# Kernel optimization log

Hardware: AMD Instinct MI355X
Metric: run time of the kernel (lower is better)

Reference implementation:

```python
import jax, jax.numpy as jnp
import numpy as np

EPS = 1e-18
MARGIN = 0.2  # hp.margin (cancels: positive/positive == 1)
BIAS = 1.0    # hp.bias


def setup_inputs() -> dict:
    key = jax.random.key(0)
    k1, k2, k3, k4 = jax.random.split(key, 4)
    B, T, D = 32, 256, 256  # T == D required by the broadcast in Ecos_sim
    return {
        "pre_VF": jax.random.normal(k1, (B, T, D), dtype=jnp.float32),
        "pre_AF": jax.random.normal(k2, (B, T, D), dtype=jnp.float32),
        "back_VF": jax.random.normal(k3, (B, T, D), dtype=jnp.float32),
        "back_AF": jax.random.normal(k4, (B, T, D), dtype=jnp.float32),
    }


def _direction_loss(V, A):
    """For each anchor i: log(1 + sum_{j != i} exp(sim(V_i, A_j))).

    sim(V_i, A_j)[t, s] = (V_i @ A_j.T)[t, s] / (||V_i||_F * colnorm(A_j)[s])
    (faithful to Ecos_sim: scalar Frobenius norm for V, per-column norm for A,
    broadcast along the last axis; positive/positive == 1 exactly, so the
    positive term and margin cancel.)
    """
    B = V.shape[0]
    # upper[i,j,t,s] = <V[i,t,:], A[j,s,:]>
    upper = jnp.einsum("itd,jsd->ijts", V, A)
    v_norm = jnp.sqrt(jnp.sum(V ** 2, axis=(1, 2)) + EPS)      # [B]
    a_norm = jnp.sqrt(jnp.sum(A ** 2, axis=1) + EPS)           # [B, D]
    sim = upper / (v_norm[:, None, None, None] * a_norm[None, :, None, :])
    e_sim = jnp.exp(sim)                                        # [B,B,T,T]
    idx = jnp.arange(B)
    down = e_sim.sum(axis=1) - e_sim[idx, idx]                  # exclude j == i
    rows = jnp.log(1.0 + down)                                  # [B,T,T]
    return rows.reshape(-1, rows.shape[-1])                     # cat along dim 0


def reference(pre_VF, pre_AF, back_VF, back_AF):
    sim_back_V = _direction_loss(back_VF, back_AF)
    sim_back_A = _direction_loss(back_AF, back_VF)
    return -(1.0 / BIAS) * (sim_back_V + sim_back_A)
```

## Files before the change

kernel.cpp:

```cpp
#include <hip/hip_runtime.h>
#include <cstdint>

#define R_TOT 8192
#define KD    256
#define SLOT  ((size_t)R_TOT * KD)
#define IVN_OFF  0
#define ICN_OFF  256
#define CSQ_OFF  (ICN_OFF + 65536)
#define MATS_OFF (CSQ_OFF + 524288)

typedef float f32x4 __attribute__((ext_vector_type(4)));
typedef int   i32x4 __attribute__((ext_vector_type(4)));
typedef int   i32x8 __attribute__((ext_vector_type(8)));

__device__ __forceinline__ void glds16(const void* g, void* l){
  __builtin_amdgcn_global_load_lds((const __attribute__((address_space(1))) uint32_t*)g,
                                   (__attribute__((address_space(3))) uint32_t*)l, 16, 0, 0);
}

__global__ void cast_ns_k(const float* __restrict__ V, const float* __restrict__ A,
                          unsigned char* __restrict__ mats, float* __restrict__ csq){
  const int tc = blockIdx.x, j = blockIdx.y, ten = blockIdx.z;
  const int tid = threadIdx.x;
  const int g    = tid & 31;
  const int tsub = tid >> 5;
  const int c    = g >> 1;
  const int half = g & 1;
  const float* X = (ten ? A : V) + (size_t)j * 65536;
  unsigned char* M = mats + (size_t)ten * SLOT + (size_t)j * 65536;
  float cs[8];
  #pragma unroll
  for (int e = 0; e < 8; ++e) cs[e] = 0.f;
  #pragma unroll
  for (int tt = 0; tt < 4; ++tt){
    const int t = tc * 32 + tt * 8 + tsub;
    const float4 p0 = *(const float4*)(X + t * 256 + g * 8);
    const float4 p1 = *(const float4*)(X + t * 256 + g * 8 + 4);
    cs[0] += p0.x * p0.x; cs[1] += p0.y * p0.y; cs[2] += p0.z * p0.z; cs[3] += p0.w * p0.w;
    cs[4] += p1.x * p1.x; cs[5] += p1.y * p1.y; cs[6] += p1.z * p1.z; cs[7] += p1.w * p1.w;
    int d0 = __builtin_amdgcn_cvt_pk_fp8_f32(p0.x, p0.y, 0, false);
    d0     = __builtin_amdgcn_cvt_pk_fp8_f32(p0.z, p0.w, d0, true);
    int d1 = __builtin_amdgcn_cvt_pk_fp8_f32(p1.x, p1.y, 0, false);
    d1     = __builtin_amdgcn_cvt_pk_fp8_f32(p1.z, p1.w, d1, true);
    int2 o; o.x = d0; o.y = d1;
    *(int2*)(M + (size_t)t * 256 + (((c ^ (t & 15)) << 4) | (half << 3))) = o;
  }
  __shared__ float red[8][256];
  #pragma unroll
  for (int e = 0; e < 8; ++e) red[tsub][g * 8 + e] = cs[e];
  __syncthreads();
  float s = 0.f;
  #pragma unroll
  for (int gg = 0; gg < 8; ++gg) s += red[gg][tid];
  csq[(size_t)((tc * 2 + ten) * 32 + j) * 256 + tid] = s;
}

__global__ void nreduce_k(const float* __restrict__ csq, float* __restrict__ ivn,
                          float* __restrict__ icn){
  const int j = blockIdx.x, ten = blockIdx.y, s = threadIdx.x;
  float c = 0.f;
  #pragma unroll
  for (int tc = 0; tc < 8; ++tc)
    c += csq[(size_t)((tc * 2 + ten) * 32 + j) * 256 + s];
  icn[ten * 8192 + j * 256 + s] = rsqrtf(c + 1e-18f);
  __shared__ float red[256];
  red[s] = c; __syncthreads();
  for (int off = 128; off > 0; off >>= 1){
    if (s < off) red[s] += red[s + off];
    __syncthreads();
  }
  if (s == 0) ivn[ten * 32 + j] = rsqrtf(red[0] + 1e-18f);
}

__global__ __launch_bounds__(512, 4) void gemm_both_k(const unsigned char* __restrict__ mats,
                                                      const float* __restrict__ ivn,
                                                      const float* __restrict__ icn,
                                                      float* __restrict__ out){
  __shared__ __align__(16) char smem[40960];
  const int tid  = threadIdx.x;
  const int lane = tid & 63;
  const int w    = tid >> 6;
  const int dir  = w >> 2;
  const int sub  = w & 3;
  const int lm   = lane & 15;
  const int kh   = lane >> 4;
  const int s0   = blockIdx.x * 16;
  const int rb   = blockIdx.y;
  const int r0   = rb * 256;
  const int ib   = rb;

  const unsigned char* rowmat = mats + (size_t)dir * SLOT;
  const unsigned char* colmat = mats + (size_t)(1 - dir) * SLOT;
  const float sivn = ivn[dir * 32 + ib] * 1.44269504088896340736f;

  char*  dbase = smem + dir * 16384;
  float* cscw  = (float*)(smem + 32768) + dir * 512;
  const unsigned char* colbase = colmat + (size_t)s0 * 256;
  const int lo16 = lane * 16;

  auto issue = [&](int x){
    const int j = x + (x >= ib ? 1 : 0);
    glds16(colbase + (size_t)j * 65536 + sub * 1024 + lo16,
           dbase + ((x & 3) << 12) + sub * 1024 + lo16);
  };

  issue(0);
  issue(1);

  {
    const float* ib2 = icn + (size_t)(1 - dir) * 8192 + s0 + lm;
    #pragma unroll
    for (int jx = 0; jx < 2; ++jx){
      const int j = sub * 8 + jx * 4 + kh;
      cscw[j * 16 + lm] = sivn * ib2[j * 256];
    }
  }

  i32x8 afr[4][2];
  #pragma unroll
  for (int mi = 0; mi < 4; ++mi){
    const unsigned char* rp = rowmat + (size_t)(r0 + sub * 64 + mi * 16 + lm) * 256;
    #pragma unroll
    for (int t = 0; t < 2; ++t){
      i32x4 lo = *(const i32x4*)(rp + ((((t << 3) | (kh << 1) | 0) ^ lm) << 4));
      i32x4 hi = *(const i32x4*)(rp + ((((t << 3) | (kh << 1) | 1) ^ lm) << 4));
      afr[mi][t] = i32x8{lo.x, lo.y, lo.z, lo.w, hi.x, hi.y, hi.z, hi.w};
    }
  }
  #pragma unroll
  for (int mi = 0; mi < 4; ++mi)
    #pragma unroll
    for (int t = 0; t < 2; ++t)
      asm volatile("" : "+v"(afr[mi][t]));

  int ad[2][2];
  #pragma unroll
  for (int t = 0; t < 2; ++t)
    #pragma unroll
    for (int u = 0; u < 2; ++u)
      ad[t][u] = lm * 256 + ((((t << 3) | (kh << 1) | u) ^ lm) << 4);

  f32x4 acc[4];
  #pragma unroll
  for (int mi = 0; mi < 4; ++mi)
    acc[mi] = f32x4{0.f, 0.f, 0.f, 0.f};
  const f32x4 fz = {0.f, 0.f, 0.f, 0.f};

  asm volatile("s_waitcnt vmcnt(0) lgkmcnt(0)" ::: "memory");
  __builtin_amdgcn_s_barrier();
  __builtin_amdgcn_sched_barrier(0);

  #pragma unroll 1
  for (int x = 0; x < 31; ++x){
    const int j = x + (x >= ib ? 1 : 0);

    if (x <= 28) issue(x + 2);

    const char* rbuf = dbase + ((x & 3) << 12);
    i32x8 b[2];
    #pragma unroll
    for (int t = 0; t < 2; ++t){
      i32x4 lo = *(const i32x4*)(rbuf + ad[t][0]);
      i32x4 hi = *(const i32x4*)(rbuf + ad[t][1]);
      b[t] = i32x8{lo.x, lo.y, lo.z, lo.w, hi.x, hi.y, hi.z, hi.w};
    }
    const float csc = cscw[j * 16 + lm];

    f32x4 S[4];
    #pragma unroll
    for (int mi = 0; mi < 4; ++mi)
      S[mi] = __builtin_amdgcn_mfma_scale_f32_16x16x128_f8f6f4(afr[mi][0], b[0], fz, 0, 0, 0, 127, 0, 127);
    #pragma unroll
    for (int mi = 0; mi < 4; ++mi)
      S[mi] = __builtin_amdgcn_mfma_scale_f32_16x16x128_f8f6f4(afr[mi][1], b[1], S[mi], 0, 0, 0, 127, 0, 127);

    #pragma unroll
    for (int mi = 0; mi < 4; ++mi){
      const f32x4 t0 = S[mi] * csc;
      f32x4 e0;
      #pragma unroll
      for (int r = 0; r < 4; ++r) e0[r] = __builtin_amdgcn_exp2f(t0[r]);
      acc[mi] += e0;
    }

    if (x <= 28)      asm volatile("s_waitcnt vmcnt(1)" ::: "memory");
    else if (x == 29) asm volatile("s_waitcnt vmcnt(0)" ::: "memory");
    if (x < 30){
      __builtin_amdgcn_s_barrier();
      __builtin_amdgcn_sched_barrier(0);
    }
  }

  __syncthreads();
  float* ebuf = (float*)smem;
  #pragma unroll
  for (int mi = 0; mi < 4; ++mi){
    #pragma unroll
    for (int r = 0; r < 4; ++r){
      const int m = sub * 64 + mi * 16 + (kh << 2) + r;
      ebuf[(dir * 256 + m) * 20 + lm] = __logf(1.f + acc[mi][r]);
    }
  }
  __syncthreads();
  #pragma unroll
  for (int p = 0; p < 2; ++p){
    const int i   = tid + p * 512;
    const int row = i >> 2;
    const int c4  = i & 3;
    const f32x4 e0 = *(const f32x4*)(&ebuf[row * 20 + c4 * 4]);
    const f32x4 e1 = *(const f32x4*)(&ebuf[(256 + row) * 20 + c4 * 4]);
    f32x4 o;
    #pragma unroll
    for (int e = 0; e < 4; ++e) o[e] = -(e0[e] + e1[e]);
    *(f32x4*)(&out[(size_t)(r0 + row) * 256 + s0 + c4 * 4]) = o;
  }
}

extern "C" void kernel_launch(void* const* d_in, const int* in_sizes, int n_in,
                              void* d_out, int out_size, void* d_ws, size_t ws_size,
                              hipStream_t stream){
  const float* V = (const float*)d_in[2];
  const float* A = (const float*)d_in[3];
  float* out = (float*)d_out;
  float* ivn = (float*)((char*)d_ws + IVN_OFF);
  float* icn = (float*)((char*)d_ws + ICN_OFF);
  float* csq = (float*)((char*)d_ws + CSQ_OFF);
  unsigned char* mats = (unsigned char*)((char*)d_ws + MATS_OFF);

  cast_ns_k<<<dim3(8, 32, 2), 256, 0, stream>>>(V, A, mats, csq);
  nreduce_k<<<dim3(32, 2), 256, 0, stream>>>(csq, ivn, icn);
  gemm_both_k<<<dim3(16, 32), 512, 0, stream>>>(mats, ivn, icn, out);
}
```

Before: 115.0 us.

## Deepen LDS ring to eight stages and process two column tiles per barrier

The shared-memory ring for column tiles grows from 4 to 8 slots, and four tiles are prefetched instead of two. The main loop now handles two tiles per iteration, with one barrier and waitcnt per pair. Within a pair, the second tile's MFMAs are interleaved with the first tile's exp/accumulate to hide latency. The cost is a larger LDS footprint (about 68KB per block), which lowers the number of blocks that can be resident per CU.

```diff
diff --git a/kernel.cpp b/kernel.cpp
--- a/kernel.cpp
+++ b/kernel.cpp
@@ -76,7 +76,7 @@
                                                       const float* __restrict__ ivn,
                                                       const float* __restrict__ icn,
                                                       float* __restrict__ out){
-  __shared__ __align__(16) char smem[40960];
+  __shared__ __align__(16) char smem[69632];
   const int tid  = threadIdx.x;
   const int lane = tid & 63;
   const int w    = tid >> 6;
@@ -93,19 +93,18 @@
   const unsigned char* colmat = mats + (size_t)(1 - dir) * SLOT;
   const float sivn = ivn[dir * 32 + ib] * 1.44269504088896340736f;
 
-  char*  dbase = smem + dir * 16384;
-  float* cscw  = (float*)(smem + 32768) + dir * 512;
+  char*  dbase = smem + dir * 32768;
+  float* cscw  = (float*)(smem + 65536) + dir * 512;
   const unsigned char* colbase = colmat + (size_t)s0 * 256;
   const int lo16 = lane * 16;
 
   auto issue = [&](int x){
     const int j = x + (x >= ib ? 1 : 0);
     glds16(colbase + (size_t)j * 65536 + sub * 1024 + lo16,
-           dbase + ((x & 3) << 12) + sub * 1024 + lo16);
+           dbase + ((x & 7) << 12) + sub * 1024 + lo16);
   };
 
-  issue(0);
-  issue(1);
+  issue(0); issue(1); issue(2); issue(3);
 
   {
     const float* ib2 = icn + (size_t)(1 - dir) * 8192 + s0 + lm;
@@ -150,46 +149,77 @@
   __builtin_amdgcn_s_barrier();
   __builtin_amdgcn_sched_barrier(0);
 
+#define RD(RX, BUF) do{                                                         \
+    i32x4 lo0_ = *(const i32x4*)((BUF) + ad[0][0]);                             \
+    i32x4 hi0_ = *(const i32x4*)((BUF) + ad[0][1]);                             \
+    i32x4 lo1_ = *(const i32x4*)((BUF) + ad[1][0]);                             \
+    i32x4 hi1_ = *(const i32x4*)((BUF) + ad[1][1]);                             \
+    RX[0] = i32x8{lo0_.x, lo0_.y, lo0_.z, lo0_.w, hi0_.x, hi0_.y, hi0_.z, hi0_.w}; \
+    RX[1] = i32x8{lo1_.x, lo1_.y, lo1_.z, lo1_.w, hi1_.x, hi1_.y, hi1_.z, hi1_.w}; \
+  }while(0)
+
+#define MFMA8(SX, BX) do{                                                       \
+    _Pragma("unroll")                                                           \
+    for (int mi_ = 0; mi_ < 4; ++mi_)                                           \
+      SX[mi_] = __builtin_amdgcn_mfma_scale_f32_16x16x128_f8f6f4(afr[mi_][0], BX[0], fz, 0, 0, 0, 127, 0, 127); \
+    _Pragma("unroll")                                                           \
+    for (int mi_ = 0; mi_ < 4; ++mi_)                                           \
+      SX[mi_] = __builtin_amdgcn_mfma_scale_f32_16x16x128_f8f6f4(afr[mi_][1], BX[1], SX[mi_], 0, 0, 0, 127, 0, 127); \
+  }while(0)
+
+#define EXPACC(SX, CY) do{                                                      \
+    _Pragma("unroll")                                                           \
+    for (int mi_ = 0; mi_ < 4; ++mi_){                                          \
+      const f32x4 t_ = SX[mi_] * (CY);                                          \
+      f32x4 e_;                                                                 \
+      _Pragma("unroll")                                                         \
+      for (int r_ = 0; r_ < 4; ++r_) e_[r_] = __builtin_amdgcn_exp2f(t_[r_]);   \
+      acc[mi_] += e_;                                                           \
+    }                                                                           \
+  }while(0)
+
+#define PAIR(xa_, xb_, NISS, VN) do{                                            \
+    const int ja_ = (xa_) + ((xa_) >= ib ? 1 : 0);                              \
+    const int jb_ = (xb_) + ((xb_) >= ib ? 1 : 0);                              \
+    const char* bufa_ = dbase + (((xa_) & 7) << 12);                            \
+    const char* bufb_ = dbase + (((xb_) & 7) << 12);                            \
+    i32x8 rA_[2], rB_[2];                                                       \
+    f32x4 S_[4];                                                                \
+    RD(rA_, bufa_);                                                             \
+    const float cA_ = cscw[ja_ * 16 + lm];                                      \
+    if ((NISS) >= 1) issue((xa_) + 4);                                          \
+    if ((NISS) >= 2) issue((xb_) + 4);                                          \
+    MFMA8(S_, rA_);                                                             \
+    RD(rB_, bufb_);                                                             \
+    const float cB_ = cscw[jb_ * 16 + lm];                                      \
+    EXPACC(S_, cA_);                                                            \
+    MFMA8(S_, rB_);                                                             \
+    EXPACC(S_, cB_);                                                            \
+    asm volatile("s_waitcnt vmcnt(" #VN ")" ::: "memory");                      \
+    __builtin_amdgcn_s_barrier();                                               \
+    __builtin_amdgcn_sched_barrier(0);                                          \
+  }while(0)
+
   #pragma unroll 1
-  for (int x = 0; x < 31; ++x){
-    const int j = x + (x >= ib ? 1 : 0);
-
-    if (x <= 28) issue(x + 2);
-
-    const char* rbuf = dbase + ((x & 3) << 12);
-    i32x8 b[2];
-    #pragma unroll
-    for (int t = 0; t < 2; ++t){
-      i32x4 lo = *(const i32x4*)(rbuf + ad[t][0]);
-      i32x4 hi = *(const i32x4*)(rbuf + ad[t][1]);
-      b[t] = i32x8{lo.x, lo.y, lo.z, lo.w, hi.x, hi.y, hi.z, hi.w};
-    }
-    const float csc = cscw[j * 16 + lm];
-
-    f32x4 S[4];
-    #pragma unroll
-    for (int mi = 0; mi < 4; ++mi)
-      S[mi] = __builtin_amdgcn_mfma_scale_f32_16x16x128_f8f6f4(afr[mi][0], b[0], fz, 0, 0, 0, 127, 0, 127);
-    #pragma unroll
-    for (int mi = 0; mi < 4; ++mi)
-      S[mi] = __builtin_amdgcn_mfma_scale_f32_16x16x128_f8f6f4(afr[mi][1], b[1], S[mi], 0, 0, 0, 127, 0, 127);
-
-    #pragma unroll
-    for (int mi = 0; mi < 4; ++mi){
-      const f32x4 t0 = S[mi] * csc;
-      f32x4 e0;
-      #pragma unroll
-      for (int r = 0; r < 4; ++r) e0[r] = __builtin_amdgcn_exp2f(t0[r]);
-      acc[mi] += e0;
-    }
-
-    if (x <= 28)      asm volatile("s_waitcnt vmcnt(1)" ::: "memory");
-    else if (x == 29) asm volatile("s_waitcnt vmcnt(0)" ::: "memory");
-    if (x < 30){
-      __builtin_amdgcn_s_barrier();
-      __builtin_amdgcn_sched_barrier(0);
-    }
-  }
+  for (int k = 0; k < 13; ++k)
+    PAIR(2 * k, 2 * k + 1, 2, 2);
+  PAIR(26, 27, 1, 1);
+  PAIR(28, 29, 0, 0);
+  {
+    const int j30 = 30 + (30 >= ib ? 1 : 0);
+    const char* buf_ = dbase + ((30 & 7) << 12);
+    i32x8 r_[2];
+    f32x4 S_[4];
+    RD(r_, buf_);
+    const float c_ = cscw[j30 * 16 + lm];
+    MFMA8(S_, r_);
+    EXPACC(S_, c_);
+  }
+
+#undef PAIR
+#undef EXPACC
+#undef MFMA8
+#undef RD
 
   __syncthreads();
   float* ebuf = (float*)smem;
```

New measurement: 154.2 us. 34.2% more time.
